# Optimization experiments

Measured on AMD Instinct MI355X. Metric: run time of the kernel, lower is better.

The kernel has to match this reference:

```python
import jax, jax.numpy as jnp
import numpy as np

N = 50000          # nodes
E = 800000         # edges (avg degree 16)
NS = 0.01          # LeakyReLU negative slope
N_CONVS = 3


def setup_inputs() -> dict:
    key = jax.random.key(0)
    ks = jax.random.split(key, 12)
    g = lambda k, s: (jax.random.normal(k, s, dtype=jnp.float32) * 0.05)
    return dict(
        x=jax.random.normal(ks[0], (N, 16), dtype=jnp.float32),
        edge_index=jax.random.randint(ks[1], (2, E), 0, N),
        edge_weight=jax.random.uniform(ks[2], (E, 1), dtype=jnp.float32),
        # prep MLP: Linear(16,64)+LeakyReLU, Linear(64,64)+Tanh
        Wp_in=g(ks[3], (16, 64)), bp_in=jnp.zeros((64,), jnp.float32),
        Wp_h=g(ks[4], (64, 64)), bp_h=jnp.zeros((64,), jnp.float32),
        # per-conv edge projection Linear(edge_dim=1, 64), stacked over 3 convs
        We=g(ks[5], (N_CONVS, 1, 64)), be=jnp.zeros((N_CONVS, 64), jnp.float32),
        # per-conv nn MLP: Linear(64,64)+LeakyReLU, Linear(64,64)+Tanh
        Wm0=g(ks[6], (N_CONVS, 64, 64)), bm0=jnp.zeros((N_CONVS, 64), jnp.float32),
        Wm1=g(ks[7], (N_CONVS, 64, 64)), bm1=jnp.zeros((N_CONVS, 64), jnp.float32),
        # post MLP: Linear(64,64)+LeakyReLU, Linear(64,32)+Tanh
        Wq0=g(ks[8], (64, 64)), bq0=jnp.zeros((64,), jnp.float32),
        Wq1=g(ks[9], (64, 32)), bq1=jnp.zeros((32,), jnp.float32),
    )


def reference(x, edge_index, edge_weight,
              Wp_in, bp_in, Wp_h, bp_h,
              We, be, Wm0, bm0, Wm1, bm1,
              Wq0, bq0, Wq1, bq1):
    lrelu = lambda v: jax.nn.leaky_relu(v, NS)
    # prep MLP (dropout=0 -> no-op)
    h = lrelu(x @ Wp_in + bp_in)
    h = jnp.tanh(h @ Wp_h + bp_h)
    src, dst = edge_index[0], edge_index[1]
    # stacked GINEConv layers (eps=0): out = nn(x + sum_j ReLU(x_j + lin_e(e_ij)))
    for k in range(N_CONVS):
        e = edge_weight @ We[k] + be[k]              # [E,64] edge embedding
        msg = jax.nn.relu(h[src] + e)                # [E,64] gather + fuse
        agg = jax.ops.segment_sum(msg, dst, num_segments=N)  # [N,64] scatter-sum
        z = agg + h                                  # (1+eps)*x with eps=0
        z = lrelu(z @ Wm0[k] + bm0[k])
        h = jnp.tanh(z @ Wm1[k] + bm1[k])
    # post MLP
    z = lrelu(h @ Wq0 + bq0)
    return jnp.tanh(z @ Wq1 + bq1)                   # [N,32]
```

## Files before the change

kernel.cpp:

```cpp
#include <hip/hip_runtime.h>
#include <hip/hip_fp16.h>
#include <math.h>

#define NS 0.01f
#define CAP 48
#define QS (1.f / 65535.f)
#define POISON 0xAAAAAAAAu

__device__ __forceinline__ float lrelu(float v) { return fmaxf(v, NS * v); }

__device__ __forceinline__ unsigned rel_cnt(unsigned raw) {
    return min(raw, raw - POISON);
}

__global__ void __launch_bounds__(512) build_kernel(
    const int* __restrict__ src, const int* __restrict__ dst,
    const float* __restrict__ ew, int* __restrict__ cnt,
    unsigned* __restrict__ bucket, int E, int fillBlocks,
    const float* __restrict__ x,
    const float* __restrict__ Wp_in, const float* __restrict__ bp_in,
    const float* __restrict__ Wp_h,  const float* __restrict__ bp_h,
    __half* __restrict__ h, int N, int prepBlocks,
    const float* __restrict__ Wm0, const float* __restrict__ Wm1,
    const float* __restrict__ Wq0, const float* __restrict__ Wq1,
    float* __restrict__ WT)
{
    __shared__ float zt[64 * 65];
    const int b = (int)blockIdx.x;
    const int t = threadIdx.x;

    if (b < fillBlocks) {
        const int e0 = (b * 512 + t) * 4;
        if (e0 + 3 < E && (E & 3) == 0) {
            const int4   d4 = *(const int4*)(dst + e0);
            const int4   s4 = *(const int4*)(src + e0);
            const float4 w4 = *(const float4*)(ew + e0);
            const int   dd[4] = {d4.x, d4.y, d4.z, d4.w};
            const int   ss[4] = {s4.x, s4.y, s4.z, s4.w};
            const float ww[4] = {w4.x, w4.y, w4.z, w4.w};
            unsigned p[4];
            #pragma unroll
            for (int q = 0; q < 4; ++q)
                p[q] = rel_cnt((unsigned)atomicAdd(&cnt[dd[q]], 1));
            #pragma unroll
            for (int q = 0; q < 4; ++q) {
                if (p[q] < CAP) {
                    const unsigned qq = __float2uint_rn(ww[q] * 65535.f) & 0xffffu;
                    __builtin_nontemporal_store(((unsigned)ss[q] << 16) | qq,
                                                &bucket[(size_t)dd[q] * CAP + p[q]]);
                }
            }
        } else {
            for (int e = e0; e < min(e0 + 4, E); ++e) {
                const int d = dst[e];
                const unsigned p = rel_cnt((unsigned)atomicAdd(&cnt[d], 1));
                if (p < CAP) {
                    const unsigned q = __float2uint_rn(ew[e] * 65535.f) & 0xffffu;
                    bucket[(size_t)d * CAP + p] = ((unsigned)src[e] << 16) | q;
                }
            }
        }
        return;
    }
    if (b < fillBlocks + prepBlocks) {
        const int n0 = (b - fillBlocks) * 64;
        #pragma unroll
        for (int r = 0; r < 2; ++r) {
            const int idx = r * 512 + t;
            const int nl = idx >> 4, i = idx & 15;
            const int n = n0 + nl;
            zt[nl * 65 + i] = (n < N) ? x[(size_t)n * 16 + i] : 0.f;
        }
        __syncthreads();
        const int lane = t & 63;
        const int w = __builtin_amdgcn_readfirstlane(t >> 6);
        float zx[16];
        #pragma unroll
        for (int i = 0; i < 16; ++i) zx[i] = zt[lane * 65 + i];
        float y[8];
        #pragma unroll
        for (int jj = 0; jj < 8; ++jj) {
            const int j = w * 8 + jj;
            float a = bp_in[j];
            #pragma unroll
            for (int i = 0; i < 16; ++i) a = fmaf(zx[i], Wp_in[i * 64 + j], a);
            y[jj] = lrelu(a);
        }
        __syncthreads();
        #pragma unroll
        for (int jj = 0; jj < 8; ++jj) zt[lane * 65 + w * 8 + jj] = y[jj];
        __syncthreads();
        #pragma unroll
        for (int jj = 0; jj < 8; ++jj) y[jj] = bp_h[w * 8 + jj];
        #pragma unroll
        for (int half = 0; half < 2; ++half) {
            float zh[32];
            #pragma unroll
            for (int i = 0; i < 32; ++i) zh[i] = zt[lane * 65 + half * 32 + i];
            #pragma unroll
            for (int jj = 0; jj < 8; ++jj) {
                const int j = w * 8 + jj;
                #pragma unroll
                for (int i = 0; i < 32; ++i)
                    y[jj] = fmaf(zh[i], Wp_h[(half * 32 + i) * 64 + j], y[jj]);
            }
        }
        __syncthreads();
        #pragma unroll
        for (int jj = 0; jj < 8; ++jj) zt[lane * 65 + w * 8 + jj] = tanhf(y[jj]);
        __syncthreads();
        #pragma unroll
        for (int r = 0; r < 8; ++r) {
            const int idx = r * 512 + t;
            const int nl = idx >> 6, i = idx & 63;
            const int n = n0 + nl;
            if (n < N) h[(size_t)n * 64 + i] = __float2half(zt[nl * 65 + i]);
        }
        return;
    }
    const int o = (b - fillBlocks - prepBlocks) * 512 + t;
    if (o >= 30720) return;
    float v;
    int d = o;
    if (d < 12288) {
        const int k = d >> 12, r = d & 4095, j = r >> 6, i = r & 63;
        v = Wm0[k * 4096 + i * 64 + j];
    } else if ((d -= 12288) < 12288) {
        const int k = d >> 12, r = d & 4095, j = r >> 6, i = r & 63;
        v = Wm1[k * 4096 + i * 64 + j];
    } else if ((d -= 12288) < 4096) {
        const int j = d >> 6, i = d & 63;
        v = Wq0[i * 64 + j];
    } else {
        d -= 4096;
        const int j = d >> 6, i = d & 63;
        v = Wq1[i * 32 + j];
    }
    WT[o] = v;
}

__device__ __forceinline__ void layer64s(float* zt, int lane, int w,
                                         const float* __restrict__ WT,
                                         const float* __restrict__ bias, int act)
{
    float y[8];
    #pragma unroll
    for (int jj = 0; jj < 8; ++jj) y[jj] = bias[w * 8 + jj];
    #pragma unroll
    for (int half = 0; half < 2; ++half) {
        float zh[32];
        #pragma unroll
        for (int i = 0; i < 32; ++i) zh[i] = zt[lane * 65 + half * 32 + i];
        #pragma unroll
        for (int jj = 0; jj < 8; ++jj) {
            const float* wr = WT + (w * 8 + jj) * 64 + half * 32;
            #pragma unroll
            for (int i = 0; i < 32; ++i) y[jj] = fmaf(zh[i], wr[i], y[jj]);
        }
    }
    __syncthreads();
    #pragma unroll
    for (int jj = 0; jj < 8; ++jj)
        zt[lane * 65 + w * 8 + jj] = act ? lrelu(y[jj]) : tanhf(y[jj]);
    __syncthreads();
}

__global__ void __launch_bounds__(512, 8) fused_conv_kernel(
    const __half* __restrict__ hin,
    const int* __restrict__ cnt,
    const unsigned* __restrict__ bucket,
    const float* __restrict__ We_k, const float* __restrict__ be_k,
    const float* __restrict__ W0T, const float* __restrict__ b0,
    const float* __restrict__ W1T, const float* __restrict__ b1,
    const float* __restrict__ Wq0T, const float* __restrict__ bq0,
    const float* __restrict__ Wq1T, const float* __restrict__ bq1,
    int do_post, __half* __restrict__ hout, float* __restrict__ out, int N)
{
    __shared__ float zt[64 * 65];
    const int t = threadIdx.x;
    const int lane = t & 63;
    const int w = __builtin_amdgcn_readfirstlane(t >> 6);
    const int n0 = (int)blockIdx.x * 64;
    const float wej = We_k[lane], bej = be_k[lane];
    const float wqs = wej * QS;

    float acc[8];
    int   len[8];
    const int nb = n0 + w * 8;
    #pragma unroll
    for (int s = 0; s < 8; ++s) {
        const int n = nb + s;
        if (n < N) {
            acc[s] = __half2float(hin[(size_t)n * 64 + lane]);
            len[s] = __builtin_amdgcn_readfirstlane(
                         (int)min(rel_cnt((unsigned)cnt[n]), (unsigned)CAP));
        } else { acc[s] = 0.f; len[s] = 0; }
    }
    const unsigned* rows = bucket + (size_t)nb * CAP;

    int m[4];
    int maxLen = 0;
    #pragma unroll
    for (int pr = 0; pr < 4; ++pr) {
        m[pr] = max(len[2 * pr], len[2 * pr + 1]);
        maxLen = max(maxLen, m[pr]);
    }
    for (int p = 0; p < maxLen; p += 8) {
        #pragma unroll
        for (int pr = 0; pr < 4; ++pr) {
            if (p < m[pr]) {
                const uint4* rA = (const uint4*)(rows + (2 * pr) * CAP);
                const uint4* rB = (const uint4*)(rows + (2 * pr + 1) * CAP);
                const uint4 a0 = rA[p >> 2], a1 = rA[(p >> 2) + 1];
                const uint4 b0_ = rB[p >> 2], b1_ = rB[(p >> 2) + 1];
                unsigned rs[16];
                rs[0] = __builtin_amdgcn_readfirstlane(a0.x);
                rs[1] = __builtin_amdgcn_readfirstlane(a0.y);
                rs[2] = __builtin_amdgcn_readfirstlane(a0.z);
                rs[3] = __builtin_amdgcn_readfirstlane(a0.w);
                rs[4] = __builtin_amdgcn_readfirstlane(a1.x);
                rs[5] = __builtin_amdgcn_readfirstlane(a1.y);
                rs[6] = __builtin_amdgcn_readfirstlane(a1.z);
                rs[7] = __builtin_amdgcn_readfirstlane(a1.w);
                rs[8]  = __builtin_amdgcn_readfirstlane(b0_.x);
                rs[9]  = __builtin_amdgcn_readfirstlane(b0_.y);
                rs[10] = __builtin_amdgcn_readfirstlane(b0_.z);
                rs[11] = __builtin_amdgcn_readfirstlane(b0_.w);
                rs[12] = __builtin_amdgcn_readfirstlane(b1_.x);
                rs[13] = __builtin_amdgcn_readfirstlane(b1_.y);
                rs[14] = __builtin_amdgcn_readfirstlane(b1_.z);
                rs[15] = __builtin_amdgcn_readfirstlane(b1_.w);
                float g[16];
                #pragma unroll
                for (int i = 0; i < 16; ++i)
                    g[i] = __half2float(hin[(size_t)(rs[i] >> 16) * 64 + lane]);
                #pragma unroll
                for (int ss = 0; ss < 2; ++ss) {
                    const int s = 2 * pr + ss;
                    #pragma unroll
                    for (int q = 0; q < 8; ++q) {
                        const float ef = fmaf((float)(rs[ss * 8 + q] & 0xffffu), wqs, bej);
                        const float v  = fmaxf(g[ss * 8 + q] + ef, 0.f);
                        acc[s] += (p + q < len[s]) ? v : 0.f;
                    }
                }
            }
        }
    }
    #pragma unroll
    for (int s = 0; s < 8; ++s)
        zt[(w * 8 + s) * 65 + lane] = acc[s];
    __syncthreads();

    layer64s(zt, lane, w, W0T, b0, 1);
    layer64s(zt, lane, w, W1T, b1, 0);

    if (!do_post) {
        #pragma unroll
        for (int r = 0; r < 8; ++r) {
            const int idx = r * 512 + t;
            const int nl = idx >> 6, i = idx & 63;
            const int n = n0 + nl;
            if (n < N) hout[(size_t)n * 64 + i] = __float2half(zt[nl * 65 + i]);
        }
        return;
    }
    layer64s(zt, lane, w, Wq0T, bq0, 1);
    {
        float y[4];
        #pragma unroll
        for (int jj = 0; jj < 4; ++jj) y[jj] = bq1[w * 4 + jj];
        #pragma unroll
        for (int half = 0; half < 2; ++half) {
            float zh[32];
            #pragma unroll
            for (int i = 0; i < 32; ++i) zh[i] = zt[lane * 65 + half * 32 + i];
            #pragma unroll
            for (int jj = 0; jj < 4; ++jj) {
                const float* wr = Wq1T + (w * 4 + jj) * 64 + half * 32;
                #pragma unroll
                for (int i = 0; i < 32; ++i) y[jj] = fmaf(zh[i], wr[i], y[jj]);
            }
        }
        __syncthreads();
        #pragma unroll
        for (int jj = 0; jj < 4; ++jj) zt[lane * 65 + w * 4 + jj] = tanhf(y[jj]);
        __syncthreads();
    }
    #pragma unroll
    for (int r = 0; r < 4; ++r) {
        const int idx = r * 512 + t;
        const int nl = idx >> 5, i = idx & 31;
        const int n = n0 + nl;
        if (n < N) out[(size_t)n * 32 + i] = zt[nl * 65 + i];
    }
}

extern "C" void kernel_launch(void* const* d_in, const int* in_sizes, int n_in,
                              void* d_out, int out_size, void* d_ws, size_t ws_size,
                              hipStream_t stream) {
    const float* x     = (const float*)d_in[0];
    const int*   ei    = (const int*)d_in[1];
    const float* ew    = (const float*)d_in[2];
    const float* Wp_in = (const float*)d_in[3];
    const float* bp_in = (const float*)d_in[4];
    const float* Wp_h  = (const float*)d_in[5];
    const float* bp_h  = (const float*)d_in[6];
    const float* We    = (const float*)d_in[7];
    const float* be    = (const float*)d_in[8];
    const float* Wm0   = (const float*)d_in[9];
    const float* bm0   = (const float*)d_in[10];
    const float* Wm1   = (const float*)d_in[11];
    const float* bm1   = (const float*)d_in[12];
    const float* Wq0   = (const float*)d_in[13];
    const float* bq0   = (const float*)d_in[14];
    const float* Wq1   = (const float*)d_in[15];
    const float* bq1   = (const float*)d_in[16];
    float* out = (float*)d_out;

    const int N = in_sizes[0] / 16;
    const int E = in_sizes[2];
    const int* src = ei;
    const int* dst = ei + E;

    __half*   hA     = (__half*)d_ws;
    __half*   hB     = hA + (size_t)N * 64;
    unsigned* bucket = (unsigned*)(hB + (size_t)N * 64);
    int*      cnt    = (int*)(bucket + (size_t)N * CAP);
    float*    WT     = (float*)(cnt + N);
    float* Wm0T   = WT;
    float* Wm1T   = Wm0T + 12288;
    float* Wq0T   = Wm1T + 12288;
    float* Wq1T   = Wq0T + 4096;

    const int fillBlocks = (E + 2047) / 2048;
    const int prepBlocks = (N + 63) / 64;
    const int wtBlocks   = (30720 + 511) / 512;
    const int tileBlocks = (N + 63) / 64;

    build_kernel<<<fillBlocks + prepBlocks + wtBlocks, 512, 0, stream>>>(
        src, dst, ew, cnt, bucket, E, fillBlocks,
        x, Wp_in, bp_in, Wp_h, bp_h, hA, N, prepBlocks,
        Wm0, Wm1, Wq0, Wq1, WT);

    fused_conv_kernel<<<tileBlocks, 512, 0, stream>>>(
        hA, cnt, bucket, We + 0 * 64, be + 0 * 64,
        Wm0T + 0 * 4096, bm0 + 0 * 64, Wm1T + 0 * 4096, bm1 + 0 * 64,
        Wq0T, bq0, Wq1T, bq1, 0, hB, out, N);
    fused_conv_kernel<<<tileBlocks, 512, 0, stream>>>(
        hB, cnt, bucket, We + 1 * 64, be + 1 * 64,
        Wm0T + 1 * 4096, bm0 + 1 * 64, Wm1T + 1 * 4096, bm1 + 1 * 64,
        Wq0T, bq0, Wq1T, bq1, 0, hA, out, N);
    fused_conv_kernel<<<tileBlocks, 512, 0, stream>>>(
        hA, cnt, bucket, We + 2 * 64, be + 2 * 64,
        Wm0T + 2 * 4096, bm0 + 2 * 64, Wm1T + 2 * 4096, bm1 + 2 * 64,
        Wq0T, bq0, Wq1T, bq1, 1, hB, out, N);
}
```

Measured before the change: 298.1 us.

## Run per-node MLP layers on MFMA with split-fp16 activations and fp16 weights

Replaces the scalar FMA 64x64 dense layers in the fused conv kernel with MFMA 16x16x32 f16 instructions. Activations are stored in shared memory as hi/lo fp16 pairs to keep near-fp32 precision, and the weights are pre-converted to fp16 in the build kernel. This targets the FMA-bound MLP portion of each conv. It also vectorizes the hidden-state output stores. The trade-offs are reduced weight precision and twice the shared memory footprint for the double buffers.

```diff
diff --git a/kernel.cpp b/kernel.cpp
--- a/kernel.cpp
+++ b/kernel.cpp
@@ -6,6 +6,11 @@
 #define CAP 48
 #define QS (1.f / 65535.f)
 #define POISON 0xAAAAAAAAu
+#define ZS 72
+
+typedef _Float16 f16;
+typedef __attribute__((ext_vector_type(8))) f16 f16x8;
+typedef __attribute__((ext_vector_type(4))) float f32x4;
 
 __device__ __forceinline__ float lrelu(float v) { return fmaxf(v, NS * v); }
 
@@ -23,7 +28,7 @@
     __half* __restrict__ h, int N, int prepBlocks,
     const float* __restrict__ Wm0, const float* __restrict__ Wm1,
     const float* __restrict__ Wq0, const float* __restrict__ Wq1,
-    float* __restrict__ WT)
+    __half* __restrict__ WTh)
 {
     __shared__ float zt[64 * 65];
     const int b = (int)blockIdx.x;
@@ -136,33 +141,47 @@
         const int j = d >> 6, i = d & 63;
         v = Wq1[i * 32 + j];
     }
-    WT[o] = v;
-}
-
-__device__ __forceinline__ void layer64s(float* zt, int lane, int w,
-                                         const float* __restrict__ WT,
-                                         const float* __restrict__ bias, int act)
+    WTh[o] = __float2half(v);
+}
+
+template<int ACT , int WLO >
+__device__ __forceinline__ void mfma_layer64(
+    const f16* __restrict__ inH, const f16* __restrict__ inL,
+    const __half* __restrict__ WTh, const float* __restrict__ bias,
+    int lane, int w, f16* __restrict__ outH, f16* __restrict__ outL)
 {
-    float y[8];
+    const int m   = w >> 1;
+    const int nb0 = (w & 1) * 2;
+    const int ar  = lane & 15;
+    const int kg  = lane >> 4;
+    const f16* ia = inH + (16 * m + ar) * ZS + kg * 8;
+    const f16* il = inL + (16 * m + ar) * ZS + kg * 8;
+    const f16x8 aH0 = *(const f16x8*)(ia);
+    const f16x8 aH1 = *(const f16x8*)(ia + 32);
+    const f16x8 aL0 = *(const f16x8*)(il);
+    const f16x8 aL1 = *(const f16x8*)(il + 32);
     #pragma unroll
-    for (int jj = 0; jj < 8; ++jj) y[jj] = bias[w * 8 + jj];
-    #pragma unroll
-    for (int half = 0; half < 2; ++half) {
-        float zh[32];
-        #pragma unroll
-        for (int i = 0; i < 32; ++i) zh[i] = zt[lane * 65 + half * 32 + i];
-        #pragma unroll
-        for (int jj = 0; jj < 8; ++jj) {
-            const float* wr = WT + (w * 8 + jj) * 64 + half * 32;
-            #pragma unroll
-            for (int i = 0; i < 32; ++i) y[jj] = fmaf(zh[i], wr[i], y[jj]);
-        }
-    }
-    __syncthreads();
-    #pragma unroll
-    for (int jj = 0; jj < 8; ++jj)
-        zt[lane * 65 + w * 8 + jj] = act ? lrelu(y[jj]) : tanhf(y[jj]);
-    __syncthreads();
+    for (int tt = 0; tt < 2; ++tt) {
+        const int nb = nb0 + tt;
+        const f16* wb = (const f16*)WTh + (16 * nb + ar) * 64 + kg * 8;
+        const f16x8 b0 = *(const f16x8*)(wb);
+        const f16x8 b1 = *(const f16x8*)(wb + 32);
+        f32x4 c = {0.f, 0.f, 0.f, 0.f};
+        c = __builtin_amdgcn_mfma_f32_16x16x32_f16(aH0, b0, c, 0, 0, 0);
+        c = __builtin_amdgcn_mfma_f32_16x16x32_f16(aH1, b1, c, 0, 0, 0);
+        c = __builtin_amdgcn_mfma_f32_16x16x32_f16(aL0, b0, c, 0, 0, 0);
+        c = __builtin_amdgcn_mfma_f32_16x16x32_f16(aL1, b1, c, 0, 0, 0);
+        const float bj = bias[16 * nb + ar];
+        #pragma unroll
+        for (int r = 0; r < 4; ++r) {
+            float y = c[r] + bj;
+            y = ACT ? lrelu(y) : tanhf(y);
+            const int row = 16 * m + kg * 4 + r;
+            const f16 hi = (f16)y;
+            outH[row * ZS + 16 * nb + ar] = hi;
+            if (WLO) outL[row * ZS + 16 * nb + ar] = (f16)(y - (float)hi);
+        }
+    }
 }
 
 __global__ void __launch_bounds__(512, 8) fused_conv_kernel(
@@ -170,13 +189,16 @@
     const int* __restrict__ cnt,
     const unsigned* __restrict__ bucket,
     const float* __restrict__ We_k, const float* __restrict__ be_k,
-    const float* __restrict__ W0T, const float* __restrict__ b0,
-    const float* __restrict__ W1T, const float* __restrict__ b1,
-    const float* __restrict__ Wq0T, const float* __restrict__ bq0,
-    const float* __restrict__ Wq1T, const float* __restrict__ bq1,
+    const __half* __restrict__ W0Th, const float* __restrict__ b0,
+    const __half* __restrict__ W1Th, const float* __restrict__ b1,
+    const __half* __restrict__ Wq0Th, const float* __restrict__ bq0,
+    const __half* __restrict__ Wq1Th, const float* __restrict__ bq1,
     int do_post, __half* __restrict__ hout, float* __restrict__ out, int N)
 {
-    __shared__ float zt[64 * 65];
+    __shared__ __align__(16) f16 bAH[64 * ZS];
+    __shared__ __align__(16) f16 bAL[64 * ZS];
+    __shared__ __align__(16) f16 bBH[64 * ZS];
+    __shared__ __align__(16) f16 bBL[64 * ZS];
     const int t = threadIdx.x;
     const int lane = t & 63;
     const int w = __builtin_amdgcn_readfirstlane(t >> 6);
@@ -186,17 +208,17 @@
 
     float acc[8];
     int   len[8];
-    const int nb = n0 + w * 8;
+    const int nb_ = n0 + w * 8;
     #pragma unroll
     for (int s = 0; s < 8; ++s) {
-        const int n = nb + s;
+        const int n = nb_ + s;
         if (n < N) {
             acc[s] = __half2float(hin[(size_t)n * 64 + lane]);
             len[s] = __builtin_amdgcn_readfirstlane(
                          (int)min(rel_cnt((unsigned)cnt[n]), (unsigned)CAP));
         } else { acc[s] = 0.f; len[s] = 0; }
     }
-    const unsigned* rows = bucket + (size_t)nb * CAP;
+    const unsigned* rows = bucket + (size_t)nb_ * CAP;
 
     int m[4];
     int maxLen = 0;
@@ -248,51 +270,57 @@
         }
     }
     #pragma unroll
-    for (int s = 0; s < 8; ++s)
-        zt[(w * 8 + s) * 65 + lane] = acc[s];
+    for (int s = 0; s < 8; ++s) {
+        const float a = acc[s];
+        const f16 hi = (f16)a;
+        bAH[(w * 8 + s) * ZS + lane] = hi;
+        bAL[(w * 8 + s) * ZS + lane] = (f16)(a - (float)hi);
+    }
     __syncthreads();
 
-    layer64s(zt, lane, w, W0T, b0, 1);
-    layer64s(zt, lane, w, W1T, b1, 0);
+    mfma_layer64<1, 1>(bAH, bAL, W0Th, b0, lane, w, bBH, bBL);
+    __syncthreads();
 
     if (!do_post) {
-        #pragma unroll
-        for (int r = 0; r < 8; ++r) {
-            const int idx = r * 512 + t;
-            const int nl = idx >> 6, i = idx & 63;
-            const int n = n0 + nl;
-            if (n < N) hout[(size_t)n * 64 + i] = __float2half(zt[nl * 65 + i]);
-        }
+        mfma_layer64<0, 0>(bBH, bBL, W1Th, b1, lane, w, bAH, bAL);
+        __syncthreads();
+        const int node = t >> 3, ch = t & 7;
+        const int n = n0 + node;
+        if (n < N)
+            *(uint4*)&hout[(size_t)n * 64 + ch * 8] =
+                *(const uint4*)&bAH[node * ZS + ch * 8];
         return;
     }
-    layer64s(zt, lane, w, Wq0T, bq0, 1);
+    mfma_layer64<0, 1>(bBH, bBL, W1Th, b1, lane, w, bAH, bAL);
+    __syncthreads();
+    mfma_layer64<1, 1>(bAH, bAL, Wq0Th, bq0, lane, w, bBH, bBL);
+    __syncthreads();
     {
-        float y[4];
-        #pragma unroll
-        for (int jj = 0; jj < 4; ++jj) y[jj] = bq1[w * 4 + jj];
-        #pragma unroll
-        for (int half = 0; half < 2; ++half) {
-            float zh[32];
-            #pragma unroll
-            for (int i = 0; i < 32; ++i) zh[i] = zt[lane * 65 + half * 32 + i];
-            #pragma unroll
-            for (int jj = 0; jj < 4; ++jj) {
-                const float* wr = Wq1T + (w * 4 + jj) * 64 + half * 32;
-                #pragma unroll
-                for (int i = 0; i < 32; ++i) y[jj] = fmaf(zh[i], wr[i], y[jj]);
-            }
-        }
-        __syncthreads();
-        #pragma unroll
-        for (int jj = 0; jj < 4; ++jj) zt[lane * 65 + w * 4 + jj] = tanhf(y[jj]);
-        __syncthreads();
-    }
-    #pragma unroll
-    for (int r = 0; r < 4; ++r) {
-        const int idx = r * 512 + t;
-        const int nl = idx >> 5, i = idx & 31;
-        const int n = n0 + nl;
-        if (n < N) out[(size_t)n * 32 + i] = zt[nl * 65 + i];
+        const int mq  = w >> 1;
+        const int nbq = w & 1;
+        const int ar  = lane & 15;
+        const int kg  = lane >> 4;
+        const f16* ia = bBH + (16 * mq + ar) * ZS + kg * 8;
+        const f16* il = bBL + (16 * mq + ar) * ZS + kg * 8;
+        const f16x8 aH0 = *(const f16x8*)(ia);
+        const f16x8 aH1 = *(const f16x8*)(ia + 32);
+        const f16x8 aL0 = *(const f16x8*)(il);
+        const f16x8 aL1 = *(const f16x8*)(il + 32);
+        const f16* wb = (const f16*)Wq1Th + (16 * nbq + ar) * 64 + kg * 8;
+        const f16x8 b0_ = *(const f16x8*)(wb);
+        const f16x8 b1_ = *(const f16x8*)(wb + 32);
+        f32x4 c = {0.f, 0.f, 0.f, 0.f};
+        c = __builtin_amdgcn_mfma_f32_16x16x32_f16(aH0, b0_, c, 0, 0, 0);
+        c = __builtin_amdgcn_mfma_f32_16x16x32_f16(aH1, b1_, c, 0, 0, 0);
+        c = __builtin_amdgcn_mfma_f32_16x16x32_f16(aL0, b0_, c, 0, 0, 0);
+        c = __builtin_amdgcn_mfma_f32_16x16x32_f16(aL1, b1_, c, 0, 0, 0);
+        const float bj = bq1[16 * nbq + ar];
+        #pragma unroll
+        for (int r = 0; r < 4; ++r) {
+            const float y = tanhf(c[r] + bj);
+            const int n = n0 + 16 * mq + kg * 4 + r;
+            if (n < N) out[(size_t)n * 32 + 16 * nbq + ar] = y;
+        }
     }
 }
 
@@ -327,11 +355,11 @@
     __half*   hB     = hA + (size_t)N * 64;
     unsigned* bucket = (unsigned*)(hB + (size_t)N * 64);
     int*      cnt    = (int*)(bucket + (size_t)N * CAP);
-    float*    WT     = (float*)(cnt + N);
-    float* Wm0T   = WT;
-    float* Wm1T   = Wm0T + 12288;
-    float* Wq0T   = Wm1T + 12288;
-    float* Wq1T   = Wq0T + 4096;
+    __half*   WTh    = (__half*)(cnt + N);
+    __half* Wm0Th = WTh;
+    __half* Wm1Th = Wm0Th + 12288;
+    __half* Wq0Th = Wm1Th + 12288;
+    __half* Wq1Th = Wq0Th + 4096;
 
     const int fillBlocks = (E + 2047) / 2048;
     const int prepBlocks = (N + 63) / 64;
@@ -341,18 +369,18 @@
     build_kernel<<<fillBlocks + prepBlocks + wtBlocks, 512, 0, stream>>>(
         src, dst, ew, cnt, bucket, E, fillBlocks,
         x, Wp_in, bp_in, Wp_h, bp_h, hA, N, prepBlocks,
-        Wm0, Wm1, Wq0, Wq1, WT);
+        Wm0, Wm1, Wq0, Wq1, WTh);
 
     fused_conv_kernel<<<tileBlocks, 512, 0, stream>>>(
         hA, cnt, bucket, We + 0 * 64, be + 0 * 64,
-        Wm0T + 0 * 4096, bm0 + 0 * 64, Wm1T + 0 * 4096, bm1 + 0 * 64,
-        Wq0T, bq0, Wq1T, bq1, 0, hB, out, N);
+        Wm0Th + 0 * 4096, bm0 + 0 * 64, Wm1Th + 0 * 4096, bm1 + 0 * 64,
+        Wq0Th, bq0, Wq1Th, bq1, 0, hB, out, N);
     fused_conv_kernel<<<tileBlocks, 512, 0, stream>>>(
         hB, cnt, bucket, We + 1 * 64, be + 1 * 64,
-        Wm0T + 1 * 4096, bm0 + 1 * 64, Wm1T + 1 * 4096, bm1 + 1 * 64,
-        Wq0T, bq0, Wq1T, bq1, 0, hA, out, N);
+        Wm0Th + 1 * 4096, bm0 + 1 * 64, Wm1Th + 1 * 4096, bm1 + 1 * 64,
+        Wq0Th, bq0, Wq1Th, bq1, 0, hA, out, N);
     fused_conv_kernel<<<tileBlocks, 512, 0, stream>>>(
         hA, cnt, bucket, We + 2 * 64, be + 2 * 64,
-        Wm0T + 2 * 4096, bm0 + 2 * 64, Wm1T + 2 * 4096, bm1 + 2 * 64,
-        Wq0T, bq0, Wq1T, bq1, 1, hB, out, N);
-}
+        Wm0Th + 2 * 4096, bm0 + 2 * 64, Wm1Th + 2 * 4096, bm1 + 2 * 64,
+        Wq0Th, bq0, Wq1Th, bq1, 1, hB, out, N);
+}
```

Measured after the change: 251.5 us. -15.6%, faster.
